# Performance work log

Hardware: AMD Instinct MI355X
Metric: run time of the kernel (lower is better)

The kernel has to match this reference:

```python
import math
import jax, jax.numpy as jnp
import numpy as np


def setup_inputs() -> dict:
    key = jax.random.key(0)
    k1, k2, k3 = jax.random.split(key, 3)
    B, CK, CV = 2, 64, 384
    T, H, W = 8, 30, 54
    N = T * H * W
    mk = jax.random.normal(k1, (B, CK, N), dtype=jnp.float32)
    qk = jax.random.normal(k2, (B, CK, H, W), dtype=jnp.float32)
    mv = jax.random.normal(k3, (B, CV, N), dtype=jnp.float32)
    return {"mk": mk, "qk": qk, "mv": mv, "topk": 20}


def _compute_affinity(mk, qk, topk):
    # mk: [B, CK, N] memory keys; qk: [B, CK, H, W] query keys
    B, CK, H, W = qk.shape
    M = H * W
    qk2 = qk.reshape(B, CK, M)                      # [B, CK, M]
    a_sq = jnp.sum(mk * mk, axis=1)[:, :, None]     # [B, N, 1]
    ab = jnp.einsum('bcn,bcm->bnm', mk, qk2)        # [B, N, M]
    affinity = (2.0 * ab - a_sq) / math.sqrt(CK)    # negative sq-distance / sqrt(CK)
    N = affinity.shape[1]
    k = min(topk, N)
    # top-k over the memory axis (dim 1): move it last for lax.top_k
    aff_t = jnp.swapaxes(affinity, 1, 2)            # [B, M, N]
    vals, idx = jax.lax.top_k(aff_t, k)             # [B, M, k]
    vals = jax.nn.softmax(vals, axis=-1)
    b_ix = jnp.arange(B)[:, None, None]
    m_ix = jnp.arange(M)[None, :, None]
    sparse = jnp.zeros_like(aff_t).at[b_ix, m_ix, idx].set(vals)  # scatter softmaxed top-k
    return jnp.swapaxes(sparse, 1, 2)               # [B, N, M]


def reference(mk, qk, mv, topk):
    affinity = _compute_affinity(mk, qk, topk)      # [B, N, M]
    mem = jnp.einsum('bcn,bnm->bcm', mv, affinity)  # propagate_feat: bmm(mv, affinity)
    return mem
```

## Files before the change

### kernel.cpp

```cpp
#include <hip/hip_runtime.h>
#include <math.h>
#include <float.h>
#include <limits.h>
#include <stdint.h>

namespace {

constexpr int B  = 2;
constexpr int CK = 64;
constexpr int N  = 12960;
constexpr int M  = 1620;
constexpr int CV = 384;
constexpr int K  = 20;

constexpr int SEGN  = 1024;
constexpr int NSEG  = (N + SEGN - 1) / SEGN;
constexpr int CAP   = 64;
constexpr int SLOTS = NSEG * CAP;
constexpr int JC    = (SLOTS + 255) / 256;
constexpr int MG    = (M + 15) / 16;
constexpr int MP    = MG * 16;

constexpr int NWG   = NSEG * MG * B;
constexpr int TXB   = (N + 63) / 64;
constexpr int TRB   = TXB * (CV / 64) * B;
constexpr int ASQB  = (B * N + 255) / 256;
constexpr int QKPB  = (B * CK * MP) / 256;

static_assert((CAP & (CAP - 1)) == 0, "CAP must be pow2");
static_assert(NSEG * SEGN >= N, "segments must cover N");
static_assert(B * CK * MP % 256 == 0, "qkpad grid exact");

__device__ __forceinline__ uint32_t f2k(float x) {
  uint32_t u = __float_as_uint(x);
  return u ^ ((u & 0x80000000u) ? 0xFFFFFFFFu : 0x80000000u);
}
__device__ __forceinline__ float k2f(uint32_t k) {
  uint32_t u = (k & 0x80000000u) ? (k ^ 0x80000000u) : ~k;
  return __uint_as_float(u);
}

__global__ __launch_bounds__(256) void prep_kernel(const float* __restrict__ mk,
                                                   const float* __restrict__ qk,
                                                   float* __restrict__ asq,
                                                   float* __restrict__ qkp) {
  const int id = blockIdx.x, t = threadIdx.x;
  if (id < ASQB) {
    int i = id * 256 + t;
    if (i >= B * N) return;
    int b = i / N, n = i - b * N;
    const float* p = mk + (size_t)b * CK * N + n;
    float s = 0.f;
#pragma unroll
    for (int c = 0; c < CK; ++c) {
      float v = p[(size_t)c * N];
      s += v * v;
    }
    asq[i] = s;
  } else {
    int i = (id - ASQB) * 256 + t;
    int row = i / MP, mp = i - row * MP;
    qkp[i] = (mp < M) ? qk[(size_t)row * M + mp] : 0.f;
  }
}

__global__ __launch_bounds__(256) void transpose_out_kernel(const float* __restrict__ outT,
                                                            float* __restrict__ out) {
  __shared__ float tile[64][65];
  int b = blockIdx.z;
  int m0 = blockIdx.x * 64;
  int c0 = blockIdx.y * 64;
  int tx = threadIdx.x & 63, ty = threadIdx.x >> 6;
  for (int r = ty; r < 64; r += 4) {
    int m = m0 + r;
    if (m < M) tile[r][tx] = outT[((size_t)b * M + m) * CV + c0 + tx];
  }
  __syncthreads();
  for (int r = ty; r < 64; r += 4) {
    int c = c0 + r, m = m0 + tx;
    if (m < M) out[((size_t)b * CV + c) * M + m] = tile[tx][r];
  }
}

template <bool FULL>
__device__ __forceinline__ void emit_round(int r, int b, int seg, int mg0, int l, int w,
                                           uint64_t lmlt,
                                           uint32_t* __restrict__ cnt,
                                           uint2* __restrict__ pairs,
                                           float (&vv)[4][SEGN]) {
  const int m = mg0 + 4 * r + w;
  if (m < M) {
    float vloc[16];
#pragma unroll
    for (int j = 0; j < 4; ++j) {
      const float4 q = *reinterpret_cast<const float4*>(&vv[w][4 * l + 256 * j]);
      vloc[4 * j + 0] = q.x;
      vloc[4 * j + 1] = q.y;
      vloc[4 * j + 2] = q.z;
      vloc[4 * j + 3] = q.w;
    }
    float a0 = fmaxf(fmaxf(vloc[0], vloc[1]), fmaxf(vloc[2], vloc[3]));
    float a1 = fmaxf(fmaxf(vloc[4], vloc[5]), fmaxf(vloc[6], vloc[7]));
    float a2 = fmaxf(fmaxf(vloc[8], vloc[9]), fmaxf(vloc[10], vloc[11]));
    float a3 = fmaxf(fmaxf(vloc[12], vloc[13]), fmaxf(vloc[14], vloc[15]));
    float s = fmaxf(fmaxf(a0, a1), fmaxf(a2, a3));
#pragma unroll
    for (int kk = 2; kk <= 64; kk <<= 1) {
#pragma unroll
      for (int jj = kk >> 1; jj > 0; jj >>= 1) {
        const float o = __shfl_xor(s, jj, 64);
        const bool keepMin = (((l & kk) == 0) == ((l & jj) == 0));
        s = keepMin ? fminf(s, o) : fmaxf(s, o);
      }
    }
    const float th = __shfl(s, 44, 64);
    const size_t pbase = ((size_t)(b * M + m) * NSEG + seg) * CAP;
    int base = 0;
#pragma unroll
    for (int r16 = 0; r16 < 16; ++r16) {
      const bool hit = vloc[r16] >= th;
      const uint64_t mask = __ballot(hit);
      if (hit) {
        const int pos = base + (int)__popcll(mask & lmlt);
        if (pos < CAP)
          pairs[pbase + pos] = make_uint2(
              f2k(vloc[r16]),
              (uint32_t)(seg * SEGN + 4 * l + 256 * (r16 >> 2) + (r16 & 3)));
      }
      base += (int)__popcll(mask);
    }
    if (l == 0)
      cnt[(size_t)(b * M + m) * NSEG + seg] = (uint32_t)(base < CAP ? base : CAP);
  }
}

template <bool FULL>
__device__ __forceinline__ void fused_body(const float* __restrict__ mk,
                                           const float* __restrict__ qkp,
                                           const float* __restrict__ asq,
                                           uint32_t* __restrict__ cnt,
                                           uint2* __restrict__ pairs,
                                           int b, int seg, int mg0,
                                           float (&vv)[4][SEGN]) {
  const int t = threadIdx.x;
  const int l = t & 63, w = t >> 6;

  const int nl0 = w * 256 + 4 * l;
  const int nb  = seg * SEGN + nl0;
  const bool vld = FULL || (nb < N);

  const float* p = mk + (size_t)b * CK * N + nb;
  const float* qrow = qkp + (size_t)b * CK * MP + mg0;

  float4 acc[16];
#pragma unroll
  for (int m = 0; m < 16; ++m) acc[m] = make_float4(0.f, 0.f, 0.f, 0.f);

  auto ld = [&](const float* q) -> float4 {
    return vld ? *reinterpret_cast<const float4*>(q) : make_float4(0.f, 0.f, 0.f, 0.f);
  };
  auto fmastep = [&](const float4& kv, const float* __restrict__ qc) {
#pragma unroll
    for (int m = 0; m < 16; ++m) {
      const float qm = qc[m];
      acc[m].x += kv.x * qm;
      acc[m].y += kv.y * qm;
      acc[m].z += kv.z * qm;
      acc[m].w += kv.w * qm;
    }
  };

  float4 kva = ld(p);
  float4 kvb = ld(p + N);
  const float* pn = p + 2 * (size_t)N;
#pragma unroll 2
  for (int c = 0; c < CK - 2; ++c) {
    const float4 kvn = ld(pn);
    pn += N;
    fmastep(kva, qrow + (size_t)c * MP);
    kva = kvb;
    kvb = kvn;
  }
  fmastep(kva, qrow + (size_t)(CK - 2) * MP);
  fmastep(kvb, qrow + (size_t)(CK - 1) * MP);

  float4 sq4 = make_float4(0.f, 0.f, 0.f, 0.f);
  if (vld) sq4 = *reinterpret_cast<const float4*>(asq + (size_t)b * N + nb);

  const uint64_t lmlt = (1ull << l) - 1ull;

#pragma unroll
  for (int r = 0; r < 4; ++r) {
#pragma unroll
    for (int mj = 0; mj < 4; ++mj) {
      const float4 a = acc[4 * r + mj];
      float4 vr;
      vr.x = (2.f * a.x - sq4.x) * 0.125f;
      vr.y = (2.f * a.y - sq4.y) * 0.125f;
      vr.z = (2.f * a.z - sq4.z) * 0.125f;
      vr.w = (2.f * a.w - sq4.w) * 0.125f;
      if (!FULL && !vld) vr = make_float4(-FLT_MAX, -FLT_MAX, -FLT_MAX, -FLT_MAX);
      *reinterpret_cast<float4*>(&vv[mj][nl0]) = vr;
    }
    __syncthreads();
    emit_round<FULL>(r, b, seg, mg0, l, w, lmlt, cnt, pairs, vv);
    __syncthreads();
  }
}

__global__ __launch_bounds__(256) void fused_tr_kernel(const float* __restrict__ mk,
                                                       const float* __restrict__ qkp,
                                                       const float* __restrict__ asq,
                                                       uint32_t* __restrict__ cnt,
                                                       uint2* __restrict__ pairs,
                                                       const float* __restrict__ mv,
                                                       float* __restrict__ mvT) {
  __shared__ __align__(16) float smem[64 * 65];

  if (blockIdx.x < NWG) {
    auto& vv = *reinterpret_cast<float(*)[4][SEGN]>(smem);
    constexpr int NX = 8;
    constexpr int Q = NWG / NX, R = NWG % NX;
    const int orig = blockIdx.x;
    const int xcd = orig & (NX - 1), idx = orig >> 3;
    const int wgid = (xcd < R ? xcd * (Q + 1) : R * (Q + 1) + (xcd - R) * Q) + idx;
    const int segb = wgid / MG;
    const int mg   = wgid - segb * MG;
    const int b    = segb / NSEG;
    const int seg  = segb - b * NSEG;
    if (seg != NSEG - 1)
      fused_body<true>(mk, qkp, asq, cnt, pairs, b, seg, mg * 16, vv);
    else
      fused_body<false>(mk, qkp, asq, cnt, pairs, b, seg, mg * 16, vv);
  } else {
    auto& tile = *reinterpret_cast<float(*)[64][65]>(smem);
    const int id = blockIdx.x - NWG;
    const int x = id % TXB;
    const int rem = id / TXB;
    const int y = rem % (CV / 64);
    const int b = rem / (CV / 64);
    const int n0 = x * 64, c0 = y * 64;
    const int tx = threadIdx.x & 63, ty = threadIdx.x >> 6;
    for (int r = ty; r < 64; r += 4) {
      int c = c0 + r, n = n0 + tx;
      tile[r][tx] = (n < N) ? mv[((size_t)b * CV + c) * N + n] : 0.f;
    }
    __syncthreads();
    for (int r = ty; r < 64; r += 4) {
      int n = n0 + r, c = c0 + tx;
      if (n < N) mvT[((size_t)b * N + n) * CV + c] = tile[tx][r];
    }
  }
}

__global__ __launch_bounds__(256) void merge_topk_gather(const uint32_t* __restrict__ cnt,
                                                         const uint2* __restrict__ pairs,
                                                         const float* __restrict__ mvT,
                                                         float* __restrict__ outT) {
  const int m = blockIdx.x, b = blockIdx.y;
  const int t = threadIdx.x;
  const int bm = b * M + m;

  __shared__ uint32_t sbase[NSEG + 1];
  constexpr int HP = 268;
  __shared__ int hist[4][HP];
  __shared__ int s_digit, s_before;
  __shared__ int wn[K];
  __shared__ uint32_t wk[K];
  __shared__ float sw[K];
  __shared__ int gcnt, ecnt, s_last;
  __shared__ int ebuf[K];
  __shared__ int rmin4[4];

  if (t < NSEG) sbase[t + 1] = cnt[(size_t)bm * NSEG + t];
  __syncthreads();
  if (t == 0) {
    sbase[0] = 0;
    uint32_t a = 0;
    for (int s = 0; s < NSEG; ++s) { a += sbase[s + 1]; sbase[s + 1] = a; }
  }
  __syncthreads();
  const int Tn = (int)sbase[NSEG];

  uint32_t k[JC];
  uint32_t nn[JC];
#pragma unroll
  for (int j = 0; j < JC; ++j) {
    int i = t + (j << 8);
    if (i < Tn) {
      int s = 0;
      while ((int)sbase[s + 1] <= i) ++s;
      uint2 pr = pairs[((size_t)bm * NSEG + s) * CAP + (i - (int)sbase[s])];
      k[j] = pr.x;
      nn[j] = pr.y;
    } else {
      k[j] = 0u;
      nn[j] = 0u;
    }
  }

  int before = 0;
  uint32_t pref = 0;
  const int w = t >> 6;
  int* myhist = &hist[w][0];

  for (int p = 0; p < 4; ++p) {
    const int s = 24 - 8 * p;
    for (int i = t; i < 4 * HP; i += 256) ((int*)hist)[i] = 0;
    __syncthreads();
    const int shHi = (p == 0) ? 0 : (s + 8);
#pragma unroll
    for (int j = 0; j < JC; ++j) {
      uint32_t key = k[j];
      bool act = (p == 0) || ((key >> shHi) == pref);
      if (act) atomicAdd(&myhist[(key >> s) & 255], 1);
    }
    __syncthreads();
    if (t < 64) {
      int d = 4 * t;
      int4 g = make_int4(0, 0, 0, 0);
#pragma unroll
      for (int ww = 0; ww < 4; ++ww) {
        int4 h = *reinterpret_cast<int4*>(&hist[ww][d]);
        g.x += h.x; g.y += h.y; g.z += h.z; g.w += h.w;
      }
      int sl = g.x + g.y + g.z + g.w;
      int sfx = sl;
#pragma unroll
      for (int off = 1; off < 64; off <<= 1) {
        int o = __shfl_down(sfx, off);
        sfx += (t + off < 64) ? o : 0;
      }
      int above = sfx - sl;
      int rem = K - before;
      if (above < rem && rem <= sfx) {
        int cum = above, ds;
        if (cum + g.w >= rem) ds = 3;
        else { cum += g.w;
          if (cum + g.z >= rem) ds = 2;
          else { cum += g.z;
            if (cum + g.y >= rem) ds = 1;
            else { cum += g.y; ds = 0; } } }
        s_digit = 4 * t + ds;
        s_before = before + cum;
      }
    }
    __syncthreads();
    pref = (pref << 8) | (uint32_t)s_digit;
    before = s_before;
  }

  const uint32_t thr = pref;
  const int need = K - before;
  if (t == 0) { gcnt = 0; ecnt = 0; }
  __syncthreads();
#pragma unroll
  for (int j = 0; j < JC; ++j) {
    uint32_t key = k[j];
    if (key > thr) {
      int q = atomicAdd(&gcnt, 1);
      wn[q] = (int)nn[j]; wk[q] = key;
    } else if (key == thr) {
      int q = atomicAdd(&ecnt, 1);
      if (q < K) ebuf[q] = (int)nn[j];
    }
  }
  __syncthreads();
  if (ecnt == need) {
    if (t < need) { wn[before + t] = ebuf[t]; wk[before + t] = thr; }
  } else {
    int last = -1;
    for (int r = 0; r < need; ++r) {
      int loc = INT_MAX;
#pragma unroll
      for (int j = 0; j < JC; ++j) {
        int n = (int)nn[j];
        if (k[j] == thr && n > last && n < loc) loc = n;
      }
#pragma unroll
      for (int off = 1; off < 64; off <<= 1) loc = min(loc, __shfl_xor(loc, off));
      if ((t & 63) == 0) rmin4[t >> 6] = loc;
      __syncthreads();
      if (t == 0) {
        int mn = min(min(rmin4[0], rmin4[1]), min(rmin4[2], rmin4[3]));
        wn[before + r] = mn; wk[before + r] = thr; s_last = mn;
      }
      __syncthreads();
      last = s_last;
    }
  }
  __syncthreads();

  if (t < 64) {
    float v = (t < K) ? k2f(wk[t]) : -FLT_MAX;
    float mx = v;
#pragma unroll
    for (int off = 1; off < 64; off <<= 1) mx = fmaxf(mx, __shfl_xor(mx, off));
    float e = (t < K) ? expf(v - mx) : 0.f;
    float ss = e;
#pragma unroll
    for (int off = 1; off < 64; off <<= 1) ss += __shfl_xor(ss, off);
    if (t < K) sw[t] = e / ss;
  }
  __syncthreads();

  if (t < CV / 4) {
    const float4* tb4 = reinterpret_cast<const float4*>(mvT + (size_t)b * N * CV);
    float4 s4 = make_float4(0.f, 0.f, 0.f, 0.f);
#pragma unroll
    for (int j = 0; j < K; ++j) {
      float wj = sw[j];
      float4 vv4 = tb4[(size_t)wn[j] * (CV / 4) + t];
      s4.x += wj * vv4.x; s4.y += wj * vv4.y; s4.z += wj * vv4.z; s4.w += wj * vv4.w;
    }
    reinterpret_cast<float4*>(outT + ((size_t)b * M + m) * CV)[t] = s4;
  }
}

}

extern "C" void kernel_launch(void* const* d_in, const int* in_sizes, int n_in,
                              void* d_out, int out_size, void* d_ws, size_t ws_size,
                              hipStream_t stream) {
  const float* mk = (const float*)d_in[0];
  const float* qk = (const float*)d_in[1];
  const float* mv = (const float*)d_in[2];
  float* out = (float*)d_out;

  char* w = (char*)d_ws;
  float* asq = (float*)w;
  size_t o = (size_t)B * N * sizeof(float);
  float* mvT = (float*)(w + o);
  o += (size_t)B * N * CV * sizeof(float);
  float* outT = (float*)(w + o);
  o += (size_t)B * M * CV * sizeof(float);
  uint32_t* cnt = (uint32_t*)(w + o);
  o += (size_t)B * M * NSEG * sizeof(uint32_t);
  uint2* pairs = (uint2*)(w + o);
  o += (size_t)B * M * NSEG * CAP * sizeof(uint2);
  float* qkp = (float*)(w + o);
  o += (size_t)B * CK * MP * sizeof(float);

  prep_kernel<<<ASQB + QKPB, 256, 0, stream>>>(mk, qk, asq, qkp);
  fused_tr_kernel<<<NWG + TRB, 256, 0, stream>>>(mk, qkp, asq, cnt, pairs, mv, mvT);
  merge_topk_gather<<<dim3(M, B), 256, 0, stream>>>(cnt, pairs, mvT, outT);
  transpose_out_kernel<<<dim3((M + 63) / 64, CV / 64, B), 256, 0, stream>>>(outT, out);
}
```

Before: 220.8 us.

## Move mv transpose into prep kernel, write output directly, remap merge blocks across XCDs

The mv transpose blocks move out of the distance/top-k kernel and into the prep kernel. The gather kernel now writes results straight into the final [B,CV,M] layout, which removes the outT buffer and the separate output transpose launch. The merge blocks are also remapped so consecutive m values land on the same XCD. In exchange, the final stores become strided with stride M, so they are uncoalesced, and the prep kernel takes on more work.

```diff
diff --git a/kernel.cpp b/kernel.cpp
--- a/kernel.cpp
+++ b/kernel.cpp
@@ -40,10 +40,13 @@
   return __uint_as_float(u);
 }
 
-__global__ __launch_bounds__(256) void prep_kernel(const float* __restrict__ mk,
-                                                   const float* __restrict__ qk,
-                                                   float* __restrict__ asq,
-                                                   float* __restrict__ qkp) {
+__global__ __launch_bounds__(256) void prep_tr_kernel(const float* __restrict__ mk,
+                                                      const float* __restrict__ qk,
+                                                      const float* __restrict__ mv,
+                                                      float* __restrict__ asq,
+                                                      float* __restrict__ qkp,
+                                                      float* __restrict__ mvT) {
+  __shared__ float tile[64][65];
   const int id = blockIdx.x, t = threadIdx.x;
   if (id < ASQB) {
     int i = id * 256 + t;
@@ -57,28 +60,27 @@
       s += v * v;
     }
     asq[i] = s;
-  } else {
+  } else if (id < ASQB + QKPB) {
     int i = (id - ASQB) * 256 + t;
     int row = i / MP, mp = i - row * MP;
     qkp[i] = (mp < M) ? qk[(size_t)row * M + mp] : 0.f;
-  }
-}
-
-__global__ __launch_bounds__(256) void transpose_out_kernel(const float* __restrict__ outT,
-                                                            float* __restrict__ out) {
-  __shared__ float tile[64][65];
-  int b = blockIdx.z;
-  int m0 = blockIdx.x * 64;
-  int c0 = blockIdx.y * 64;
-  int tx = threadIdx.x & 63, ty = threadIdx.x >> 6;
-  for (int r = ty; r < 64; r += 4) {
-    int m = m0 + r;
-    if (m < M) tile[r][tx] = outT[((size_t)b * M + m) * CV + c0 + tx];
-  }
-  __syncthreads();
-  for (int r = ty; r < 64; r += 4) {
-    int c = c0 + r, m = m0 + tx;
-    if (m < M) out[((size_t)b * CV + c) * M + m] = tile[tx][r];
+  } else {
+    const int tid = id - ASQB - QKPB;
+    const int x = tid % TXB;
+    const int rem = tid / TXB;
+    const int y = rem % (CV / 64);
+    const int b = rem / (CV / 64);
+    const int n0 = x * 64, c0 = y * 64;
+    const int tx = t & 63, ty = t >> 6;
+    for (int r = ty; r < 64; r += 4) {
+      int c = c0 + r, n = n0 + tx;
+      tile[r][tx] = (n < N) ? mv[((size_t)b * CV + c) * N + n] : 0.f;
+    }
+    __syncthreads();
+    for (int r = ty; r < 64; r += 4) {
+      int n = n0 + r, c = c0 + tx;
+      if (n < N) mvT[((size_t)b * N + n) * CV + c] = tile[tx][r];
+    }
   }
 }
 
@@ -208,56 +210,39 @@
   }
 }
 
-__global__ __launch_bounds__(256) void fused_tr_kernel(const float* __restrict__ mk,
-                                                       const float* __restrict__ qkp,
-                                                       const float* __restrict__ asq,
-                                                       uint32_t* __restrict__ cnt,
-                                                       uint2* __restrict__ pairs,
-                                                       const float* __restrict__ mv,
-                                                       float* __restrict__ mvT) {
-  __shared__ __align__(16) float smem[64 * 65];
-
-  if (blockIdx.x < NWG) {
-    auto& vv = *reinterpret_cast<float(*)[4][SEGN]>(smem);
-    constexpr int NX = 8;
-    constexpr int Q = NWG / NX, R = NWG % NX;
-    const int orig = blockIdx.x;
-    const int xcd = orig & (NX - 1), idx = orig >> 3;
-    const int wgid = (xcd < R ? xcd * (Q + 1) : R * (Q + 1) + (xcd - R) * Q) + idx;
-    const int segb = wgid / MG;
-    const int mg   = wgid - segb * MG;
-    const int b    = segb / NSEG;
-    const int seg  = segb - b * NSEG;
-    if (seg != NSEG - 1)
-      fused_body<true>(mk, qkp, asq, cnt, pairs, b, seg, mg * 16, vv);
-    else
-      fused_body<false>(mk, qkp, asq, cnt, pairs, b, seg, mg * 16, vv);
-  } else {
-    auto& tile = *reinterpret_cast<float(*)[64][65]>(smem);
-    const int id = blockIdx.x - NWG;
-    const int x = id % TXB;
-    const int rem = id / TXB;
-    const int y = rem % (CV / 64);
-    const int b = rem / (CV / 64);
-    const int n0 = x * 64, c0 = y * 64;
-    const int tx = threadIdx.x & 63, ty = threadIdx.x >> 6;
-    for (int r = ty; r < 64; r += 4) {
-      int c = c0 + r, n = n0 + tx;
-      tile[r][tx] = (n < N) ? mv[((size_t)b * CV + c) * N + n] : 0.f;
-    }
-    __syncthreads();
-    for (int r = ty; r < 64; r += 4) {
-      int n = n0 + r, c = c0 + tx;
-      if (n < N) mvT[((size_t)b * N + n) * CV + c] = tile[tx][r];
-    }
-  }
+__global__ __launch_bounds__(256) void fused_kernel(const float* __restrict__ mk,
+                                                    const float* __restrict__ qkp,
+                                                    const float* __restrict__ asq,
+                                                    uint32_t* __restrict__ cnt,
+                                                    uint2* __restrict__ pairs) {
+  __shared__ float vv[4][SEGN];
+
+  constexpr int NX = 8;
+  constexpr int Q = NWG / NX, R = NWG % NX;
+  const int orig = blockIdx.x;
+  const int xcd = orig & (NX - 1), idx = orig >> 3;
+  const int wgid = (xcd < R ? xcd * (Q + 1) : R * (Q + 1) + (xcd - R) * Q) + idx;
+  const int segb = wgid / MG;
+  const int mg   = wgid - segb * MG;
+  const int b    = segb / NSEG;
+  const int seg  = segb - b * NSEG;
+
+  if (seg != NSEG - 1)
+    fused_body<true>(mk, qkp, asq, cnt, pairs, b, seg, mg * 16, vv);
+  else
+    fused_body<false>(mk, qkp, asq, cnt, pairs, b, seg, mg * 16, vv);
 }
 
 __global__ __launch_bounds__(256) void merge_topk_gather(const uint32_t* __restrict__ cnt,
                                                          const uint2* __restrict__ pairs,
                                                          const float* __restrict__ mvT,
-                                                         float* __restrict__ outT) {
-  const int m = blockIdx.x, b = blockIdx.y;
+                                                         float* __restrict__ out) {
+  const int mb = blockIdx.x;
+  constexpr int NX = 8;
+  constexpr int MQ = M / NX, MR = M % NX;
+  const int xcd = mb & (NX - 1), idx = mb >> 3;
+  const int m = (xcd < MR ? xcd * (MQ + 1) : MR * (MQ + 1) + (xcd - MR) * MQ) + idx;
+  const int b = blockIdx.y;
   const int t = threadIdx.x;
   const int bm = b * M + m;
 
@@ -413,7 +398,11 @@
       float4 vv4 = tb4[(size_t)wn[j] * (CV / 4) + t];
       s4.x += wj * vv4.x; s4.y += wj * vv4.y; s4.z += wj * vv4.z; s4.w += wj * vv4.w;
     }
-    reinterpret_cast<float4*>(outT + ((size_t)b * M + m) * CV)[t] = s4;
+    float* ob = out + (size_t)b * CV * M + m;
+    ob[(size_t)(4 * t + 0) * M] = s4.x;
+    ob[(size_t)(4 * t + 1) * M] = s4.y;
+    ob[(size_t)(4 * t + 2) * M] = s4.z;
+    ob[(size_t)(4 * t + 3) * M] = s4.w;
   }
 }
 
@@ -432,8 +421,6 @@
   size_t o = (size_t)B * N * sizeof(float);
   float* mvT = (float*)(w + o);
   o += (size_t)B * N * CV * sizeof(float);
-  float* outT = (float*)(w + o);
-  o += (size_t)B * M * CV * sizeof(float);
   uint32_t* cnt = (uint32_t*)(w + o);
   o += (size_t)B * M * NSEG * sizeof(uint32_t);
   uint2* pairs = (uint2*)(w + o);
@@ -441,8 +428,7 @@
   float* qkp = (float*)(w + o);
   o += (size_t)B * CK * MP * sizeof(float);
 
-  prep_kernel<<<ASQB + QKPB, 256, 0, stream>>>(mk, qk, asq, qkp);
-  fused_tr_kernel<<<NWG + TRB, 256, 0, stream>>>(mk, qkp, asq, cnt, pairs, mv, mvT);
-  merge_topk_gather<<<dim3(M, B), 256, 0, stream>>>(cnt, pairs, mvT, outT);
-  transpose_out_kernel<<<dim3((M + 63) / 64, CV / 64, B), 256, 0, stream>>>(outT, out);
-}
+  prep_tr_kernel<<<ASQB + QKPB + TRB, 256, 0, stream>>>(mk, qk, mv, asq, qkp, mvT);
+  fused_kernel<<<NWG, 256, 0, stream>>>(mk, qkp, asq, cnt, pairs);
+  merge_topk_gather<<<dim3(M, B), 256, 0, stream>>>(cnt, pairs, mvT, out);
+}
```

After: 227.1 us. 2.9% more time.

## Fuse key norms and qk padding into distance kernel, drop prep launch

Applied to the files above, without the earlier changes.

Removes the separate prep kernel. Squared key norms are now accumulated inside the distance GEMM loop from the already loaded mk values, and qk is read directly with a masked tail variant in place of a padded copy. It also reorders blocks so the transpose blocks come first, and applies an XCD-aware remap to the merge kernel's m index. This trades one launch and an extra pass over mk for a few more FMAs per step and two extra template instantiations.

```diff
diff --git a/kernel.cpp b/kernel.cpp
--- a/kernel.cpp
+++ b/kernel.cpp
@@ -19,17 +19,13 @@
 constexpr int SLOTS = NSEG * CAP;
 constexpr int JC    = (SLOTS + 255) / 256;
 constexpr int MG    = (M + 15) / 16;
-constexpr int MP    = MG * 16;
 
 constexpr int NWG   = NSEG * MG * B;
 constexpr int TXB   = (N + 63) / 64;
 constexpr int TRB   = TXB * (CV / 64) * B;
-constexpr int ASQB  = (B * N + 255) / 256;
-constexpr int QKPB  = (B * CK * MP) / 256;
 
 static_assert((CAP & (CAP - 1)) == 0, "CAP must be pow2");
 static_assert(NSEG * SEGN >= N, "segments must cover N");
-static_assert(B * CK * MP % 256 == 0, "qkpad grid exact");
 
 __device__ __forceinline__ uint32_t f2k(float x) {
   uint32_t u = __float_as_uint(x);
@@ -38,30 +34,6 @@
 __device__ __forceinline__ float k2f(uint32_t k) {
   uint32_t u = (k & 0x80000000u) ? (k ^ 0x80000000u) : ~k;
   return __uint_as_float(u);
-}
-
-__global__ __launch_bounds__(256) void prep_kernel(const float* __restrict__ mk,
-                                                   const float* __restrict__ qk,
-                                                   float* __restrict__ asq,
-                                                   float* __restrict__ qkp) {
-  const int id = blockIdx.x, t = threadIdx.x;
-  if (id < ASQB) {
-    int i = id * 256 + t;
-    if (i >= B * N) return;
-    int b = i / N, n = i - b * N;
-    const float* p = mk + (size_t)b * CK * N + n;
-    float s = 0.f;
-#pragma unroll
-    for (int c = 0; c < CK; ++c) {
-      float v = p[(size_t)c * N];
-      s += v * v;
-    }
-    asq[i] = s;
-  } else {
-    int i = (id - ASQB) * 256 + t;
-    int row = i / MP, mp = i - row * MP;
-    qkp[i] = (mp < M) ? qk[(size_t)row * M + mp] : 0.f;
-  }
 }
 
 __global__ __launch_bounds__(256) void transpose_out_kernel(const float* __restrict__ outT,
@@ -134,10 +106,9 @@
   }
 }
 
-template <bool FULL>
+template <bool FULL, bool MTAIL>
 __device__ __forceinline__ void fused_body(const float* __restrict__ mk,
-                                           const float* __restrict__ qkp,
-                                           const float* __restrict__ asq,
+                                           const float* __restrict__ qk,
                                            uint32_t* __restrict__ cnt,
                                            uint2* __restrict__ pairs,
                                            int b, int seg, int mg0,
@@ -150,24 +121,31 @@
   const bool vld = FULL || (nb < N);
 
   const float* p = mk + (size_t)b * CK * N + nb;
-  const float* qrow = qkp + (size_t)b * CK * MP + mg0;
+  const float* qrow = qk + (size_t)b * CK * M + mg0;
+  const int vq = M - mg0;
 
   float4 acc[16];
 #pragma unroll
   for (int m = 0; m < 16; ++m) acc[m] = make_float4(0.f, 0.f, 0.f, 0.f);
+  float4 sqa = make_float4(0.f, 0.f, 0.f, 0.f);
 
   auto ld = [&](const float* q) -> float4 {
     return vld ? *reinterpret_cast<const float4*>(q) : make_float4(0.f, 0.f, 0.f, 0.f);
   };
-  auto fmastep = [&](const float4& kv, const float* __restrict__ qc) {
+  auto fmastep = [&](const float4& kv, int c) {
+    const float* qc = qrow + (size_t)c * M;
 #pragma unroll
     for (int m = 0; m < 16; ++m) {
-      const float qm = qc[m];
+      const float qm = (MTAIL && m >= vq) ? 0.f : qc[m];
       acc[m].x += kv.x * qm;
       acc[m].y += kv.y * qm;
       acc[m].z += kv.z * qm;
       acc[m].w += kv.w * qm;
     }
+    sqa.x += kv.x * kv.x;
+    sqa.y += kv.y * kv.y;
+    sqa.z += kv.z * kv.z;
+    sqa.w += kv.w * kv.w;
   };
 
   float4 kva = ld(p);
@@ -177,15 +155,12 @@
   for (int c = 0; c < CK - 2; ++c) {
     const float4 kvn = ld(pn);
     pn += N;
-    fmastep(kva, qrow + (size_t)c * MP);
+    fmastep(kva, c);
     kva = kvb;
     kvb = kvn;
   }
-  fmastep(kva, qrow + (size_t)(CK - 2) * MP);
-  fmastep(kvb, qrow + (size_t)(CK - 1) * MP);
-
-  float4 sq4 = make_float4(0.f, 0.f, 0.f, 0.f);
-  if (vld) sq4 = *reinterpret_cast<const float4*>(asq + (size_t)b * N + nb);
+  fmastep(kva, CK - 2);
+  fmastep(kvb, CK - 1);
 
   const uint64_t lmlt = (1ull << l) - 1ull;
 
@@ -195,10 +170,10 @@
     for (int mj = 0; mj < 4; ++mj) {
       const float4 a = acc[4 * r + mj];
       float4 vr;
-      vr.x = (2.f * a.x - sq4.x) * 0.125f;
-      vr.y = (2.f * a.y - sq4.y) * 0.125f;
-      vr.z = (2.f * a.z - sq4.z) * 0.125f;
-      vr.w = (2.f * a.w - sq4.w) * 0.125f;
+      vr.x = (2.f * a.x - sqa.x) * 0.125f;
+      vr.y = (2.f * a.y - sqa.y) * 0.125f;
+      vr.z = (2.f * a.z - sqa.z) * 0.125f;
+      vr.w = (2.f * a.w - sqa.w) * 0.125f;
       if (!FULL && !vld) vr = make_float4(-FLT_MAX, -FLT_MAX, -FLT_MAX, -FLT_MAX);
       *reinterpret_cast<float4*>(&vv[mj][nl0]) = vr;
     }
@@ -209,32 +184,16 @@
 }
 
 __global__ __launch_bounds__(256) void fused_tr_kernel(const float* __restrict__ mk,
-                                                       const float* __restrict__ qkp,
-                                                       const float* __restrict__ asq,
+                                                       const float* __restrict__ qk,
+                                                       const float* __restrict__ mv,
+                                                       float* __restrict__ mvT,
                                                        uint32_t* __restrict__ cnt,
-                                                       uint2* __restrict__ pairs,
-                                                       const float* __restrict__ mv,
-                                                       float* __restrict__ mvT) {
+                                                       uint2* __restrict__ pairs) {
   __shared__ __align__(16) float smem[64 * 65];
 
-  if (blockIdx.x < NWG) {
-    auto& vv = *reinterpret_cast<float(*)[4][SEGN]>(smem);
-    constexpr int NX = 8;
-    constexpr int Q = NWG / NX, R = NWG % NX;
-    const int orig = blockIdx.x;
-    const int xcd = orig & (NX - 1), idx = orig >> 3;
-    const int wgid = (xcd < R ? xcd * (Q + 1) : R * (Q + 1) + (xcd - R) * Q) + idx;
-    const int segb = wgid / MG;
-    const int mg   = wgid - segb * MG;
-    const int b    = segb / NSEG;
-    const int seg  = segb - b * NSEG;
-    if (seg != NSEG - 1)
-      fused_body<true>(mk, qkp, asq, cnt, pairs, b, seg, mg * 16, vv);
-    else
-      fused_body<false>(mk, qkp, asq, cnt, pairs, b, seg, mg * 16, vv);
-  } else {
+  if (blockIdx.x < TRB) {
     auto& tile = *reinterpret_cast<float(*)[64][65]>(smem);
-    const int id = blockIdx.x - NWG;
+    const int id = blockIdx.x;
     const int x = id % TXB;
     const int rem = id / TXB;
     const int y = rem % (CV / 64);
@@ -250,6 +209,25 @@
       int n = n0 + r, c = c0 + tx;
       if (n < N) mvT[((size_t)b * N + n) * CV + c] = tile[tx][r];
     }
+  } else {
+    auto& vv = *reinterpret_cast<float(*)[4][SEGN]>(smem);
+    constexpr int NX = 8;
+    constexpr int Q = NWG / NX, R = NWG % NX;
+    const int orig = blockIdx.x - TRB;
+    const int xcd = orig & (NX - 1), idx = orig >> 3;
+    const int wgid = (xcd < R ? xcd * (Q + 1) : R * (Q + 1) + (xcd - R) * Q) + idx;
+    const int segb = wgid / MG;
+    const int mg   = wgid - segb * MG;
+    const int b    = segb / NSEG;
+    const int seg  = segb - b * NSEG;
+    const int mg0  = mg * 16;
+    if (seg != NSEG - 1) {
+      if (mg != MG - 1) fused_body<true, false>(mk, qk, cnt, pairs, b, seg, mg0, vv);
+      else              fused_body<true, true >(mk, qk, cnt, pairs, b, seg, mg0, vv);
+    } else {
+      if (mg != MG - 1) fused_body<false, false>(mk, qk, cnt, pairs, b, seg, mg0, vv);
+      else              fused_body<false, true >(mk, qk, cnt, pairs, b, seg, mg0, vv);
+    }
   }
 }
 
@@ -257,7 +235,12 @@
                                                          const uint2* __restrict__ pairs,
                                                          const float* __restrict__ mvT,
                                                          float* __restrict__ outT) {
-  const int m = blockIdx.x, b = blockIdx.y;
+  const int mb = blockIdx.x;
+  constexpr int NX = 8;
+  constexpr int MQ = M / NX, MR = M % NX;
+  const int xcd = mb & (NX - 1), idx = mb >> 3;
+  const int m = (xcd < MR ? xcd * (MQ + 1) : MR * (MQ + 1) + (xcd - MR) * MQ) + idx;
+  const int b = blockIdx.y;
   const int t = threadIdx.x;
   const int bm = b * M + m;
 
@@ -428,21 +411,16 @@
   float* out = (float*)d_out;
 
   char* w = (char*)d_ws;
-  float* asq = (float*)w;
-  size_t o = (size_t)B * N * sizeof(float);
-  float* mvT = (float*)(w + o);
-  o += (size_t)B * N * CV * sizeof(float);
+  float* mvT = (float*)w;
+  size_t o = (size_t)B * N * CV * sizeof(float);
   float* outT = (float*)(w + o);
   o += (size_t)B * M * CV * sizeof(float);
   uint32_t* cnt = (uint32_t*)(w + o);
   o += (size_t)B * M * NSEG * sizeof(uint32_t);
   uint2* pairs = (uint2*)(w + o);
   o += (size_t)B * M * NSEG * CAP * sizeof(uint2);
-  float* qkp = (float*)(w + o);
-  o += (size_t)B * CK * MP * sizeof(float);
-
-  prep_kernel<<<ASQB + QKPB, 256, 0, stream>>>(mk, qk, asq, qkp);
-  fused_tr_kernel<<<NWG + TRB, 256, 0, stream>>>(mk, qkp, asq, cnt, pairs, mv, mvT);
+
+  fused_tr_kernel<<<TRB + NWG, 256, 0, stream>>>(mk, qk, mv, mvT, cnt, pairs);
   merge_topk_gather<<<dim3(M, B), 256, 0, stream>>>(cnt, pairs, mvT, outT);
   transpose_out_kernel<<<dim3((M + 63) / 64, CV / 64, B), 256, 0, stream>>>(outT, out);
 }
```

Result: slower. 227.8 us (+3.2%).
